# Kernel tuning notes

Measured on AMD Instinct MI355X. Metric: run time of the kernel, lower is better.

## Reference

```python
import jax, jax.numpy as jnp
import numpy as np

EPS = 1e-5
NEIGHBOR_K = 3
NEG_SLOPE = 0.2

def _conv(x, w):
    # x: [N,C,H,W], w: [O,I,3,3], stride 1, SAME padding
    return jax.lax.conv_general_dilated(
        x, w, window_strides=(1, 1), padding='SAME',
        dimension_numbers=('NCHW', 'OIHW', 'NCHW'))

def _bn(x, gamma, beta):
    # BatchNorm2d in training mode: batch statistics over (N,H,W), biased var
    m = x.mean(axis=(0, 2, 3), keepdims=True)
    v = x.var(axis=(0, 2, 3), keepdims=True)
    xn = (x - m) * jax.lax.rsqrt(v + EPS)
    return xn * gamma.reshape(1, -1, 1, 1) + beta.reshape(1, -1, 1, 1)

def _lrelu(x):
    return jnp.where(x >= 0, x, NEG_SLOPE * x)

def _maxpool2(x):
    return jax.lax.reduce_window(x, -jnp.inf, jax.lax.max,
                                 (1, 1, 2, 2), (1, 1, 2, 2), 'VALID')

def _features(x, w1, g1, b1, w2, g2, b2, w3, g3, b3, w4, g4, b4):
    x = _maxpool2(_lrelu(_bn(_conv(x, w1), g1, b1)))
    x = _maxpool2(_lrelu(_bn(_conv(x, w2), g2, b2)))
    x = _lrelu(_bn(_conv(x, w3), g3, b3))
    x = _lrelu(_bn(_conv(x, w4), g4, b4))
    return x  # [N, 64, 21, 21]

def setup_inputs() -> dict:
    key = jax.random.key(0)
    ks = jax.random.split(key, 8)
    inp = {
        'input1': jax.random.normal(ks[0], (32, 3, 84, 84), jnp.float32),
        'input2': jax.random.normal(ks[1], (5, 5, 3, 84, 84), jnp.float32),
        'w1': jax.random.normal(ks[2], (64, 3, 3, 3), jnp.float32) * 0.1,
        'g1': jax.random.uniform(ks[3], (64,), jnp.float32, 0.5, 1.5),
        'b1': jnp.zeros((64,), jnp.float32),
        'w2': jax.random.normal(ks[4], (64, 64, 3, 3), jnp.float32) * 0.1,
        'g2': jax.random.uniform(ks[5], (64,), jnp.float32, 0.5, 1.5),
        'b2': jnp.zeros((64,), jnp.float32),
        'w3': jax.random.normal(ks[6], (64, 64, 3, 3), jnp.float32) * 0.1,
        'g3': jax.random.uniform(ks[7], (64,), jnp.float32, 0.5, 1.5),
        'b3': jnp.zeros((64,), jnp.float32),
        'w4': jax.random.normal(jax.random.fold_in(key, 100), (64, 64, 3, 3), jnp.float32) * 0.1,
        'g4': jax.random.uniform(jax.random.fold_in(key, 101), (64,), jnp.float32, 0.5, 1.5),
        'b4': jnp.zeros((64,), jnp.float32),
    }
    return inp

def reference(input1, input2, w1, g1, b1, w2, g2, b2, w3, g3, b3, w4, g4, b4):
    params = (w1, g1, b1, w2, g2, b2, w3, g3, b3, w4, g4, b4)
    # Query features: [B, C, h, w]
    q = _features(input1, *params)
    B, C, h, w = q.shape
    hw = h * w
    Q = q.reshape(B, C, hw).transpose(0, 2, 1)            # [B, hw, C]
    qn = jnp.linalg.norm(Q, axis=2, keepdims=True)        # [B, hw, 1]
    # Support features, BN stats per class-batch (matches per-class forward)
    s = jax.vmap(lambda x: _features(x, *params))(input2) # [nc, shot, C, h, w]
    nc, shot = s.shape[0], s.shape[1]
    S = s.transpose(0, 2, 1, 3, 4).reshape(nc, C, shot * hw)  # [nc, C, M]
    sn = jnp.linalg.norm(S, axis=1, keepdims=True)            # [nc, 1, M]
    # Cosine similarities: [B, nc, hw, M]
    sims = jnp.einsum('bqc,ncm->bnqm', Q, S)
    sims = sims / (qn[:, None, :, :] * sn[None, :, :, :])
    topv = jax.lax.top_k(sims, NEIGHBOR_K)[0]              # [B, nc, hw, k]
    return topv.sum(axis=(2, 3))                           # [B, nc]
```

## Files before the change

kernel.cpp:

```cpp
#include <hip/hip_runtime.h>
#include <hip/hip_bf16.h>
#include <stdint.h>

#define NQ 32
#define NCLS 5
#define SHOT 5
#define NIMG 57
#define P1 7056
#define P2 1764
#define P3 441
#define PX 3528
#define MM (SHOT*P3)
#define EPSB 1e-5f
#define SLOPE 0.2f
#define NEGINF -3.4e38f
#define NREP 32
#define MSPAN 576
#define MRNG 4
#define SLS 88

typedef __attribute__((ext_vector_type(8))) short short8;
typedef __attribute__((ext_vector_type(4))) float f32x4;

__device__ __forceinline__ unsigned short bf16bits(float v)
{
    __hip_bfloat16 h = __float2bfloat16(v);
    return *reinterpret_cast<unsigned short*>(&h);
}
__device__ __forceinline__ float bits2f(unsigned short u)
{
    unsigned int x = ((unsigned int)u) << 16;
    return *reinterpret_cast<float*>(&x);
}

__global__ void pack_all_k(const float* __restrict__ w1, const float* __restrict__ w2,
                           const float* __restrict__ w3, const float* __restrict__ w4,
                           unsigned short* __restrict__ wpk1, unsigned short* __restrict__ wpk2,
                           unsigned short* __restrict__ wpk3, unsigned short* __restrict__ wpk4,
                           float* __restrict__ sums)
{
    int i = blockIdx.x * 256 + threadIdx.x;
    if (i < 4 * 6 * 64 * 2 * NREP) sums[i] = 0.f;
    if (i < 3 * 36864) {
        int set = i / 36864, ii = i - set * 36864;
        const float* w = (set == 0) ? w2 : (set == 1) ? w3 : w4;
        unsigned short* wpk = (set == 0) ? wpk2 : (set == 1) ? wpk3 : wpk4;
        int j = ii & 7, lane = (ii >> 3) & 63, chunk = ii >> 9;
        int nt = chunk & 3, half = (chunk >> 2) & 1, t = chunk >> 3;
        int co = nt * 16 + (lane & 15);
        int ci = half * 32 + (lane >> 4) * 8 + j;
        wpk[ii] = bf16bits(w[co * 576 + ci * 9 + t]);
    } else {
        int ii = i - 3 * 36864;
        if (ii >= 4096) return;
        int j = ii & 7, lane = (ii >> 3) & 63, c8 = ii >> 9;
        int nt = c8 & 3, f = c8 >> 2;
        int co = nt * 16 + (lane & 15), q = lane >> 4;
        int k = q * 8 + j;
        float val = 0.f;
        if (f == 0) {
            int t = k >> 2, ci = k & 3;
            if (ci < 3) val = w1[co * 27 + ci * 9 + t];
        } else if (k < 4) {
            int ci = k & 3;
            if (ci < 3) val = w1[co * 27 + ci * 9 + 8];
        }
        wpk1[ii] = bf16bits(val);
    }
}

__global__ __launch_bounds__(256) void conv1m_k(const float* __restrict__ in1,
                                                const float* __restrict__ in2,
                                                const unsigned short* __restrict__ wpk1,
                                                __hip_bfloat16* __restrict__ xpool,
                                                float* __restrict__ sums)
{
    constexpr int S = 84, P = P1, MBLK = 256, NB = 28, SPAN = MBLK + 2 * S + 2;
    __shared__ __align__(16) unsigned short ls4[SPAN * 4];
    __shared__ float qs[4][64], qs2[4][64];
    int img = blockIdx.x / NB;
    int p0 = (blockIdx.x % NB) * MBLK;
    int tid = threadIdx.x, lane = tid & 63, wv = tid >> 6;
    int col = lane & 15, quad = lane >> 4;
    const float* in = (img < NQ) ? in1 + (size_t)img * 3 * P1
                                 : in2 + (size_t)(img - NQ) * 3 * P1;
    for (int u = tid; u < SPAN; u += 256) {
        int p = p0 - S - 1 + u;
        union { unsigned short us[4]; uint2 u2; } o;
        o.u2 = (uint2){0u, 0u};
        if (p >= 0 && p < P) {
            o.us[0] = bf16bits(in[p]);
            o.us[1] = bf16bits(in[P1 + p]);
            o.us[2] = bf16bits(in[2 * P1 + p]);
        }
        *(uint2*)(ls4 + u * 4) = o.u2;
    }
    const short8* wb = (const short8*)wpk1;
    short8 b0[4], b1[4];
    #pragma unroll
    for (int nt = 0; nt < 4; ++nt) {
        b0[nt] = wb[(size_t)(nt * 64 + lane)];
        b1[nt] = wb[(size_t)((4 + nt) * 64 + lane)];
    }
    int t0 = 2 * quad, t1 = t0 + 1;
    int d0 = (t0 / 3 - 1) * S + (t0 % 3 - 1);
    int d1 = (t1 / 3 - 1) * S + (t1 % 3 - 1);
    const int d8 = S + 1;
    int tx0 = t0 % 3, tx1 = t1 % 3;
    __syncthreads();
    f32x4 acc[4][4];
    #pragma unroll
    for (int mt = 0; mt < 4; ++mt)
        #pragma unroll
        for (int nt = 0; nt < 4; ++nt) acc[mt][nt] = (f32x4){0.f, 0.f, 0.f, 0.f};
    #pragma unroll
    for (int mt = 0; mt < 4; ++mt) {
        int pl = wv * 64 + mt * 16 + col;
        int xm = (p0 + pl) % S;
        int base = pl + S + 1;
        uint2 h0 = *(const uint2*)(ls4 + (base + d0) * 4);
        uint2 h1 = *(const uint2*)(ls4 + (base + d1) * 4);
        uint2 h8 = *(const uint2*)(ls4 + (base + d8) * 4);
        bool ok0 = (tx0 == 0) ? (xm >= 1) : ((tx0 == 2) ? (xm <= S - 2) : true);
        bool ok1 = (tx1 == 0) ? (xm >= 1) : ((tx1 == 2) ? (xm <= S - 2) : true);
        bool ok8 = (quad == 0) && (xm <= S - 2);
        if (!ok0) h0 = (uint2){0u, 0u};
        if (!ok1) h1 = (uint2){0u, 0u};
        if (!ok8) h8 = (uint2){0u, 0u};
        union { uint4 u; short8 s; } ca, cb;
        ca.u = (uint4){h0.x, h0.y, h1.x, h1.y};
        cb.u = (uint4){h8.x, h8.y, 0u, 0u};
        #pragma unroll
        for (int nt = 0; nt < 4; ++nt) {
            acc[mt][nt] = __builtin_amdgcn_mfma_f32_16x16x32_bf16(ca.s, b0[nt], acc[mt][nt], 0, 0, 0);
            acc[mt][nt] = __builtin_amdgcn_mfma_f32_16x16x32_bf16(cb.s, b1[nt], acc[mt][nt], 0, 0, 0);
        }
    }
    float s[4] = {0.f, 0.f, 0.f, 0.f}, s2[4] = {0.f, 0.f, 0.f, 0.f};
    __hip_bfloat16* ob = xpool + (size_t)img * PX * 64;
    #pragma unroll
    for (int mt = 0; mt < 4; ++mt) {
        int tb = p0 + wv * 64 + mt * 16 + quad * 4;
        #pragma unroll
        for (int reg = 0; reg < 4; ++reg) {
            int pr = tb + reg;
            if (pr < P) {
                #pragma unroll
                for (int nt = 0; nt < 4; ++nt) {
                    float v = acc[mt][nt][reg];
                    s[nt] += v;
                    s2[nt] = fmaf(v, v, s2[nt]);
                }
            }
        }
        #pragma unroll
        for (int pr2 = 0; pr2 < 2; ++pr2) {
            int m0 = tb + pr2 * 2;
            if (m0 < P) {
                #pragma unroll
                for (int nt = 0; nt < 4; ++nt) {
                    float v = fmaxf(acc[mt][nt][pr2 * 2], acc[mt][nt][pr2 * 2 + 1]);
                    ob[(size_t)(m0 >> 1) * 64 + nt * 16 + col] = __float2bfloat16(v);
                }
            }
        }
    }
    #pragma unroll
    for (int d = 16; d < 64; d <<= 1)
        #pragma unroll
        for (int nt = 0; nt < 4; ++nt) {
            s[nt] += __shfl_xor(s[nt], d, 64);
            s2[nt] += __shfl_xor(s2[nt], d, 64);
        }
    if (quad == 0) {
        #pragma unroll
        for (int nt = 0; nt < 4; ++nt) {
            qs[wv][nt * 16 + col] = s[nt];
            qs2[wv][nt * 16 + col] = s2[nt];
        }
    }
    __syncthreads();
    if (wv == 0) {
        int g = (img < NQ) ? 0 : 1 + (img - NQ) / SHOT;
        int rep = blockIdx.x & (NREP - 1);
        float ts = qs[0][lane] + qs[1][lane] + qs[2][lane] + qs[3][lane];
        float ts2 = qs2[0][lane] + qs2[1][lane] + qs2[2][lane] + qs2[3][lane];
        float* base = sums + ((size_t)(g * 64 + lane) * 2) * NREP + rep;
        atomicAdd(base, ts);
        atomicAdd(base + NREP, ts2);
    }
}

template <int S, int MBLK, int MODE, bool POOLX>
__global__ __launch_bounds__(256) void conv64m_k(const unsigned short* __restrict__ inv,
                                                 const unsigned short* __restrict__ wpk,
                                                 __hip_bfloat16* __restrict__ out,
                                                 float* __restrict__ sums,
                                                 const float* __restrict__ msin)
{
    constexpr int P = S * S;
    constexpr int MT = MBLK / 64;
    constexpr int NB = (P + MBLK - 1) / MBLK;
    constexpr int SPAN = MBLK + 2 * S + 2;
    __shared__ __align__(16) unsigned short ls[SPAN * 72];
    __shared__ float qs[4][64], qs2[4][64];
    int img = blockIdx.x / NB;
    int p0 = (blockIdx.x % NB) * MBLK;
    int tid = threadIdx.x;
    int lane = tid & 63, wv = tid >> 6;
    int col = lane & 15, quad = lane >> 4;
    int g = (img < NQ) ? 0 : 1 + (img - NQ) / SHOT;
    if constexpr (MODE == 0) {
        const unsigned short* ib = inv + (size_t)img * P * 64;
        for (int u = tid; u < SPAN * 8; u += 256) {
            int pix = u >> 3, part = u & 7;
            int p = p0 - S - 1 + pix;
            short8 v = {0, 0, 0, 0, 0, 0, 0, 0};
            if (p >= 0 && p < P) v = *(const short8*)(ib + (size_t)p * 64 + part * 8);
            *(short8*)(ls + pix * 72 + part * 8) = v;
        }
    } else {
        int part = tid & 7;
        float ba[8], bb[8];
        #pragma unroll
        for (int j = 0; j < 8; ++j) {
            float2 ab = ((const float2*)msin)[g * 64 + part * 8 + j];
            ba[j] = ab.x;
            bb[j] = ab.y;
        }
        if constexpr (MODE == 1) {
            const unsigned short* ib = inv + (size_t)img * P * 64;
            for (int u = tid; u < SPAN * 8; u += 256) {
                int pix = u >> 3;
                int p = p0 - S - 1 + pix;
                union { unsigned short us[8]; short8 s8; } o;
                #pragma unroll
                for (int j = 0; j < 8; ++j) o.us[j] = 0;
                if (p >= 0 && p < P) {
                    union { short8 s8; unsigned short us[8]; } x;
                    x.s8 = *(const short8*)(ib + (size_t)p * 64 + part * 8);
                    #pragma unroll
                    for (int j = 0; j < 8; ++j) {
                        float v = fmaf(bits2f(x.us[j]), ba[j], bb[j]);
                        v = fmaxf(v, SLOPE * v);
                        o.us[j] = bf16bits(v);
                    }
                }
                *(short8*)(ls + pix * 72 + part * 8) = o.s8;
            }
        } else {
            const unsigned short* ib2 = inv + (size_t)img * (2 * (size_t)P) * 64;
            for (int u = tid; u < SPAN * 8; u += 256) {
                int pix = u >> 3;
                int p = p0 - S - 1 + pix;
                union { unsigned short us[8]; short8 s8; } o;
                #pragma unroll
                for (int j = 0; j < 8; ++j) o.us[j] = 0;
                if (p >= 0 && p < P) {
                    int y = p / S, x = p - y * S;
                    const unsigned short* src = ib2 + ((size_t)(2 * y) * S + x) * 64 + part * 8;
                    union { short8 s8; unsigned short us[8]; } x0, x1;
                    x0.s8 = *(const short8*)src;
                    x1.s8 = *(const short8*)(src + (size_t)S * 64);
                    #pragma unroll
                    for (int j = 0; j < 8; ++j) {
                        float v = fmaxf(bits2f(x0.us[j]), bits2f(x1.us[j]));
                        v = fmaf(v, ba[j], bb[j]);
                        v = fmaxf(v, SLOPE * v);
                        o.us[j] = bf16bits(v);
                    }
                }
                *(short8*)(ls + pix * 72 + part * 8) = o.s8;
            }
        }
    }
    __syncthreads();
    f32x4 acc[MT][4];
    #pragma unroll
    for (int mt = 0; mt < MT; ++mt)
        #pragma unroll
        for (int nt = 0; nt < 4; ++nt) acc[mt][nt] = (f32x4){0.f, 0.f, 0.f, 0.f};
    bool mok0[MT], mok2[MT];
    #pragma unroll
    for (int mt = 0; mt < MT; ++mt) {
        int xm = (p0 + wv * (MT * 16) + mt * 16 + col) % S;
        mok0[mt] = xm >= 1;
        mok2[mt] = xm <= S - 2;
    }
    const short8* wb = (const short8*)wpk;
    #pragma unroll
    for (int ky = 0; ky < 3; ++ky) {
        #pragma unroll
        for (int kx = 0; kx < 3; ++kx) {
            int t = ky * 3 + kx;
            int d = (ky - 1) * S + (kx - 1);
            #pragma unroll
            for (int half = 0; half < 2; ++half) {
                short8 b[4];
                #pragma unroll
                for (int nt = 0; nt < 4; ++nt)
                    b[nt] = wb[((t * 2 + half) * 4 + nt) * 64 + lane];
                #pragma unroll
                for (int mt = 0; mt < MT; ++mt) {
                    int idx = wv * (MT * 16) + mt * 16 + col + S + 1 + d;
                    short8 a = *(const short8*)(ls + idx * 72 + half * 32 + quad * 8);
                    bool ok = (kx == 0) ? mok0[mt] : (kx == 2) ? mok2[mt] : true;
                    if (!ok) a = (short8){0, 0, 0, 0, 0, 0, 0, 0};
                    #pragma unroll
                    for (int nt = 0; nt < 4; ++nt)
                        acc[mt][nt] = __builtin_amdgcn_mfma_f32_16x16x32_bf16(a, b[nt], acc[mt][nt], 0, 0, 0);
                }
            }
        }
    }
    float s[4] = {0.f, 0.f, 0.f, 0.f}, s2[4] = {0.f, 0.f, 0.f, 0.f};
    __hip_bfloat16* ob = out + (size_t)img * (POOLX ? P / 2 : P) * 64;
    #pragma unroll
    for (int mt = 0; mt < MT; ++mt) {
        int tb = p0 + wv * (MT * 16) + mt * 16 + quad * 4;
        #pragma unroll
        for (int reg = 0; reg < 4; ++reg) {
            int pr = tb + reg;
            if (pr < P) {
                #pragma unroll
                for (int nt = 0; nt < 4; ++nt) {
                    float v = acc[mt][nt][reg];
                    s[nt] += v;
                    s2[nt] = fmaf(v, v, s2[nt]);
                }
            }
        }
        if constexpr (POOLX) {
            #pragma unroll
            for (int pr2 = 0; pr2 < 2; ++pr2) {
                int m0 = tb + pr2 * 2;
                if (m0 < P) {
                    #pragma unroll
                    for (int nt = 0; nt < 4; ++nt) {
                        float v = fmaxf(acc[mt][nt][pr2 * 2], acc[mt][nt][pr2 * 2 + 1]);
                        ob[(size_t)(m0 >> 1) * 64 + nt * 16 + col] = __float2bfloat16(v);
                    }
                }
            }
        } else {
            #pragma unroll
            for (int reg = 0; reg < 4; ++reg) {
                int pr = tb + reg;
                if (pr < P) {
                    #pragma unroll
                    for (int nt = 0; nt < 4; ++nt)
                        ob[(size_t)pr * 64 + nt * 16 + col] = __float2bfloat16(acc[mt][nt][reg]);
                }
            }
        }
    }
    #pragma unroll
    for (int d = 16; d < 64; d <<= 1)
        #pragma unroll
        for (int nt = 0; nt < 4; ++nt) {
            s[nt] += __shfl_xor(s[nt], d, 64);
            s2[nt] += __shfl_xor(s2[nt], d, 64);
        }
    if (quad == 0) {
        #pragma unroll
        for (int nt = 0; nt < 4; ++nt) {
            qs[wv][nt * 16 + col] = s[nt];
            qs2[wv][nt * 16 + col] = s2[nt];
        }
    }
    __syncthreads();
    if (wv == 0) {
        int rep = blockIdx.x & (NREP - 1);
        float ts = qs[0][lane] + qs[1][lane] + qs[2][lane] + qs[3][lane];
        float ts2 = qs2[0][lane] + qs2[1][lane] + qs2[2][lane] + qs2[3][lane];
        float* base = sums + ((size_t)(g * 64 + lane) * 2) * NREP + rep;
        atomicAdd(base, ts);
        atomicAdd(base + NREP, ts2);
    }
}

__global__ void finalize_k(const float* __restrict__ sums, float* __restrict__ ms,
                           const float* __restrict__ gamma, const float* __restrict__ beta, int P)
{
    int i = blockIdx.x * blockDim.x + threadIdx.x;
    if (i >= 6 * 64) return;
    int g = i >> 6, c = i & 63;
    const float* ps = sums + (size_t)i * 2 * NREP;
    float s = 0.f, s2 = 0.f;
    #pragma unroll
    for (int r = 0; r < NREP; ++r) { s += ps[r]; s2 += ps[NREP + r]; }
    float cnt = (float)((g == 0 ? NQ : SHOT) * P);
    float mean = s / cnt;
    float var = s2 / cnt - mean * mean;
    float a = rsqrtf(var + EPSB) * gamma[c];
    ms[i * 2] = a;
    ms[i * 2 + 1] = fmaf(-mean, a, beta[c]);
}

__global__ __launch_bounds__(256) void bnnorm_k(const unsigned short* __restrict__ x,
                                                const float* __restrict__ ms,
                                                __hip_bfloat16* __restrict__ out)
{
    int lane = threadIdx.x & 63, wvr = threadIdx.x >> 6;
    int pix = blockIdx.x * 4 + wvr;
    if (pix >= NIMG * P3) return;
    int img = pix / P3;
    int g = (img < NQ) ? 0 : 1 + (img - NQ) / SHOT;
    float v = fmaf(bits2f(x[(size_t)pix * 64 + lane]), ms[(g * 64 + lane) * 2], ms[(g * 64 + lane) * 2 + 1]);
    v = v >= 0.f ? v : SLOPE * v;
    float ss = v * v;
    #pragma unroll
    for (int d = 32; d > 0; d >>= 1) ss += __shfl_xor(ss, d, 64);
    out[(size_t)pix * 64 + lane] = __float2bfloat16(v * rsqrtf(ss));
}

__device__ __forceinline__ void ins3(float v, float& t0, float& t1, float& t2)
{
    float n1 = __builtin_amdgcn_fmed3f(v, t0, t1);
    float n2 = __builtin_amdgcn_fmed3f(v, t1, t2);
    t0 = fmaxf(t0, v);
    t1 = n1;
    t2 = n2;
}

__global__ __launch_bounds__(256, 6) void sim_part_k(const __hip_bfloat16* __restrict__ fhat,
                                                     float* __restrict__ part)
{
    __shared__ __align__(16) unsigned short sl[64 * SLS];
    int t = blockIdx.x;
    int mr = t & 3;
    int qb = (t >> 2) % 7;
    int n = (t / 28) % NCLS;
    int bq = t / (28 * NCLS);
    int tid = threadIdx.x, lane = tid & 63, wv = tid >> 6;
    int col = lane & 15, quad = lane >> 4;
    int q = qb * 64 + wv * 16 + col;
    int qc = q < P3 ? q : P3 - 1;
    const unsigned short* qp = (const unsigned short*)fhat + ((size_t)bq * P3 + qc) * 64;
    short8 a0 = *(const short8*)(qp + quad * 8);
    short8 a1 = *(const short8*)(qp + 32 + quad * 8);
    const unsigned short* sp = (const unsigned short*)fhat + (size_t)(NQ + n * SHOT) * P3 * 64;
    int m_lo = mr * MSPAN;
    int m_cnt = MM - m_lo; if (m_cnt > MSPAN) m_cnt = MSPAN;
    int nch = (m_cnt + 63) >> 6;
    float t0[4], t1[4], t2[4];
    #pragma unroll
    for (int r = 0; r < 4; ++r) { t0[r] = NEGINF; t1[r] = NEGINF; t2[r] = NEGINF; }
    int srow = tid >> 3, scc = (tid & 7) * 8;
    for (int c = 0; c < nch; ++c) {
        int m0 = m_lo + c * 64;
        __syncthreads();
        #pragma unroll
        for (int pass = 0; pass < 2; ++pass) {
            int row = srow + pass * 32;
            int m = m0 + row;
            short8 vv = {0, 0, 0, 0, 0, 0, 0, 0};
            if (m < MM) vv = *(const short8*)(sp + (size_t)m * 64 + scc);
            *(short8*)(sl + row * SLS + scc) = vv;
        }
        __syncthreads();
        const unsigned short* sr = sl + col * SLS + quad * 8;
        #pragma unroll
        for (int mt = 0; mt < 4; ++mt) {
            if (m0 + mt * 16 < MM) {
                short8 b0 = *(const short8*)(sr);
                short8 b1 = *(const short8*)(sr + 32);
                f32x4 acc = {0.f, 0.f, 0.f, 0.f};
                acc = __builtin_amdgcn_mfma_f32_16x16x32_bf16(a0, b0, acc, 0, 0, 0);
                acc = __builtin_amdgcn_mfma_f32_16x16x32_bf16(a1, b1, acc, 0, 0, 0);
                #pragma unroll
                for (int r = 0; r < 4; ++r) ins3(acc[r], t0[r], t1[r], t2[r]);
            }
            sr += 16 * SLS;
        }
    }
    #pragma unroll
    for (int d = 1; d < 16; d <<= 1)
        #pragma unroll
        for (int r = 0; r < 4; ++r) {
            float u0 = __shfl_xor(t0[r], d, 64);
            float u1 = __shfl_xor(t1[r], d, 64);
            float u2 = __shfl_xor(t2[r], d, 64);
            ins3(u0, t0[r], t1[r], t2[r]);
            ins3(u1, t0[r], t1[r], t2[r]);
            ins3(u2, t0[r], t1[r], t2[r]);
        }
    if (col == 0) {
        #pragma unroll
        for (int r = 0; r < 4; ++r) {
            int ql = wv * 16 + quad * 4 + r;
            float* pp = part + ((((size_t)(bq * NCLS + n) * 7 + qb) * 4 + mr) * 64 + ql) * 3;
            pp[0] = t0[r];
            pp[1] = t1[r];
            pp[2] = t2[r];
        }
    }
}

__global__ __launch_bounds__(256) void sim_merge_k(const float* __restrict__ part,
                                                   float* __restrict__ out)
{
    __shared__ float red[4];
    int b = blockIdx.x;
    int tid = threadIdx.x, lane = tid & 63, wv = tid >> 6;
    float s = 0.f;
    for (int q = tid; q < P3; q += 256) {
        int qb = q >> 6, ql = q & 63;
        const float* pp = part + (((size_t)b * 7 + qb) * 4 * 64 + ql) * 3;
        float v0 = pp[0], v1 = pp[1], v2 = pp[2];
        #pragma unroll
        for (int mr = 1; mr < 4; ++mr) {
            const float* pm = pp + (size_t)mr * 192;
            ins3(pm[0], v0, v1, v2);
            ins3(pm[1], v0, v1, v2);
            ins3(pm[2], v0, v1, v2);
        }
        s += v0 + v1 + v2;
    }
    #pragma unroll
    for (int d = 32; d > 0; d >>= 1) s += __shfl_xor(s, d, 64);
    if (lane == 0) red[wv] = s;
    __syncthreads();
    if (tid == 0) out[b] = red[0] + red[1] + red[2] + red[3];
}

extern "C" void kernel_launch(void* const* d_in, const int* in_sizes, int n_in,
                              void* d_out, int out_size, void* d_ws, size_t ws_size,
                              hipStream_t stream)
{
    const float* input1 = (const float*)d_in[0];
    const float* input2 = (const float*)d_in[1];
    const float* w1 = (const float*)d_in[2];
    const float* g1 = (const float*)d_in[3];
    const float* b1 = (const float*)d_in[4];
    const float* w2 = (const float*)d_in[5];
    const float* g2 = (const float*)d_in[6];
    const float* b2 = (const float*)d_in[7];
    const float* w3 = (const float*)d_in[8];
    const float* g3 = (const float*)d_in[9];
    const float* b3 = (const float*)d_in[10];
    const float* w4 = (const float*)d_in[11];
    const float* g4 = (const float*)d_in[12];
    const float* b4 = (const float*)d_in[13];
    float* out = (float*)d_out;

    char* w8 = (char*)d_ws;
    const size_t oB = 51480576;
    const size_t oT = oB + 12870144;
    const size_t STG = 6 * 64 * 2 * NREP * sizeof(float);
    __hip_bfloat16* xpool1 = (__hip_bfloat16*)(w8 + 0);
    __hip_bfloat16* conv3raw = (__hip_bfloat16*)(w8 + 0);
    __hip_bfloat16* conv4raw = (__hip_bfloat16*)(w8 + 9652608);
    __hip_bfloat16* fhat = (__hip_bfloat16*)(w8 + 16087680);
    __hip_bfloat16* xpool2 = (__hip_bfloat16*)(w8 + oB);
    float* sums = (float*)(w8 + oT);
    float* ms = (float*)(w8 + oT + 4 * STG);
    unsigned short* wpk2 = (unsigned short*)(w8 + oT + 4 * STG + 12288);
    unsigned short* wpk3 = (unsigned short*)(w8 + oT + 4 * STG + 12288 + 73728);
    unsigned short* wpk4 = (unsigned short*)(w8 + oT + 4 * STG + 12288 + 147456);
    unsigned short* wpk1 = (unsigned short*)(w8 + oT + 4 * STG + 12288 + 221184);
    const size_t oP = oT + 4 * STG + 12288 + 221184 + 8192;
    float* part = (float*)(w8 + oP);
    if (ws_size < oP + (size_t)NQ * NCLS * 7 * MRNG * 64 * 3 * sizeof(float)) return;
    float* sums1 = sums;
    float* sums2 = sums + 6 * 64 * 2 * NREP;
    float* sums3 = sums2 + 6 * 64 * 2 * NREP;
    float* sums4 = sums3 + 6 * 64 * 2 * NREP;

    pack_all_k<<<448, 256, 0, stream>>>(w1, w2, w3, w4, wpk1, wpk2, wpk3, wpk4, sums);

    conv1m_k<<<NIMG * 28, 256, 0, stream>>>(input1, input2, wpk1, xpool1, sums1);
    finalize_k<<<2, 256, 0, stream>>>(sums1, ms + 0, g1, b1, P1);
    conv64m_k<42, 256, 2, true><<<NIMG * 7, 256, 0, stream>>>(
        (const unsigned short*)xpool1, wpk2, xpool2, sums2, ms + 0);
    finalize_k<<<2, 256, 0, stream>>>(sums2, ms + 768, g2, b2, P2);
    conv64m_k<21, 128, 2, false><<<NIMG * 4, 256, 0, stream>>>(
        (const unsigned short*)xpool2, wpk3, conv3raw, sums3, ms + 768);
    finalize_k<<<2, 256, 0, stream>>>(sums3, ms + 1536, g3, b3, P3);
    conv64m_k<21, 128, 1, false><<<NIMG * 4, 256, 0, stream>>>(
        (const unsigned short*)conv3raw, wpk4, conv4raw, sums4, ms + 1536);
    finalize_k<<<2, 256, 0, stream>>>(sums4, ms + 2304, g4, b4, P3);
    bnnorm_k<<<6285, 256, 0, stream>>>((const unsigned short*)conv4raw, ms + 2304, fhat);
    sim_part_k<<<NQ * NCLS * 7 * MRNG, 256, 0, stream>>>(fhat, part);
    sim_merge_k<<<NQ * NCLS, 256, 0, stream>>>(part, out);
}
```

Measured before the change: 222.0 us.

## Widen similarity query tile to 128 rows, prefetch support chunks, swizzle top-k merge

The similarity kernel now gives each wave two 16-row query groups (128 queries per block instead of 64). Each support tile loaded into LDS therefore feeds twice as many MFMAs, and there are fewer blocks (4 query blocks instead of 7). Support rows for the next chunk are prefetched into registers while the current chunk is computed, and the LDS row stride shrinks to 72. The cross-lane top-3 merge switches from shfl_xor to ds_swizzle, and ins3 drops two temporaries. Register pressure rises (launch bound goes from 6 to 5 waves), and the last query block pads 128 rows for only 441 queries.

Result: no change. 224.2 us (+1.0%).

```diff
diff --git a/kernel.cpp b/kernel.cpp
--- a/kernel.cpp
+++ b/kernel.cpp
@@ -17,7 +17,9 @@
 #define NREP 32
 #define MSPAN 576
 #define MRNG 4
-#define SLS 88
+#define QBLK 128
+#define NQB 4
+#define SLS 72
 
 typedef __attribute__((ext_vector_type(8))) short short8;
 typedef __attribute__((ext_vector_type(4))) float f32x4;
@@ -416,84 +418,109 @@
 
 __device__ __forceinline__ void ins3(float v, float& t0, float& t1, float& t2)
 {
-    float n1 = __builtin_amdgcn_fmed3f(v, t0, t1);
-    float n2 = __builtin_amdgcn_fmed3f(v, t1, t2);
+    t2 = __builtin_amdgcn_fmed3f(v, t1, t2);
+    t1 = __builtin_amdgcn_fmed3f(v, t0, t1);
     t0 = fmaxf(t0, v);
-    t1 = n1;
-    t2 = n2;
-}
-
-__global__ __launch_bounds__(256, 6) void sim_part_k(const __hip_bfloat16* __restrict__ fhat,
+}
+
+template <int PAT>
+__device__ __forceinline__ void swzmerge(float& t0, float& t1, float& t2)
+{
+    float u0 = __int_as_float(__builtin_amdgcn_ds_swizzle(__float_as_int(t0), PAT));
+    float u1 = __int_as_float(__builtin_amdgcn_ds_swizzle(__float_as_int(t1), PAT));
+    float u2 = __int_as_float(__builtin_amdgcn_ds_swizzle(__float_as_int(t2), PAT));
+    ins3(u0, t0, t1, t2);
+    ins3(u1, t0, t1, t2);
+    ins3(u2, t0, t1, t2);
+}
+
+__global__ __launch_bounds__(256, 5) void sim_part_k(const __hip_bfloat16* __restrict__ fhat,
                                                      float* __restrict__ part)
 {
     __shared__ __align__(16) unsigned short sl[64 * SLS];
     int t = blockIdx.x;
     int mr = t & 3;
-    int qb = (t >> 2) % 7;
-    int n = (t / 28) % NCLS;
-    int bq = t / (28 * NCLS);
+    int qb = (t >> 2) & 3;
+    int n = (t >> 4) % NCLS;
+    int bq = t / (16 * NCLS);
     int tid = threadIdx.x, lane = tid & 63, wv = tid >> 6;
     int col = lane & 15, quad = lane >> 4;
-    int q = qb * 64 + wv * 16 + col;
-    int qc = q < P3 ? q : P3 - 1;
-    const unsigned short* qp = (const unsigned short*)fhat + ((size_t)bq * P3 + qc) * 64;
-    short8 a0 = *(const short8*)(qp + quad * 8);
-    short8 a1 = *(const short8*)(qp + 32 + quad * 8);
+    short8 a0[2], a1[2];
+    #pragma unroll
+    for (int g = 0; g < 2; ++g) {
+        int q = qb * QBLK + wv * 32 + g * 16 + col;
+        int qc = q < P3 ? q : P3 - 1;
+        const unsigned short* qp = (const unsigned short*)fhat + ((size_t)bq * P3 + qc) * 64;
+        a0[g] = *(const short8*)(qp + quad * 8);
+        a1[g] = *(const short8*)(qp + 32 + quad * 8);
+    }
     const unsigned short* sp = (const unsigned short*)fhat + (size_t)(NQ + n * SHOT) * P3 * 64;
     int m_lo = mr * MSPAN;
     int m_cnt = MM - m_lo; if (m_cnt > MSPAN) m_cnt = MSPAN;
     int nch = (m_cnt + 63) >> 6;
-    float t0[4], t1[4], t2[4];
-    #pragma unroll
-    for (int r = 0; r < 4; ++r) { t0[r] = NEGINF; t1[r] = NEGINF; t2[r] = NEGINF; }
+    float t0[2][4], t1[2][4], t2[2][4];
+    #pragma unroll
+    for (int g = 0; g < 2; ++g)
+        #pragma unroll
+        for (int r = 0; r < 4; ++r) { t0[g][r] = NEGINF; t1[g][r] = NEGINF; t2[g][r] = NEGINF; }
     int srow = tid >> 3, scc = (tid & 7) * 8;
+    const unsigned short* gp = sp + (size_t)(m_lo + srow) * 64 + scc;
+    unsigned short* ld0 = sl + srow * SLS + scc;
+    const unsigned short* sr = sl + col * SLS + quad * 8;
+    int mcur = m_lo + srow;
+    const short8 z8 = {0, 0, 0, 0, 0, 0, 0, 0};
+    short8 v0 = z8, v1 = z8;
+    if (mcur < MM) v0 = *(const short8*)gp;
+    if (mcur + 32 < MM) v1 = *(const short8*)(gp + 32 * 64);
     for (int c = 0; c < nch; ++c) {
+        __syncthreads();
+        *(short8*)ld0 = v0;
+        *(short8*)(ld0 + 32 * SLS) = v1;
+        __syncthreads();
+        if (c + 1 < nch) {
+            gp += 64 * 64;
+            mcur += 64;
+            v0 = z8; v1 = z8;
+            if (mcur < MM) v0 = *(const short8*)gp;
+            if (mcur + 32 < MM) v1 = *(const short8*)(gp + 32 * 64);
+        }
         int m0 = m_lo + c * 64;
-        __syncthreads();
-        #pragma unroll
-        for (int pass = 0; pass < 2; ++pass) {
-            int row = srow + pass * 32;
-            int m = m0 + row;
-            short8 vv = {0, 0, 0, 0, 0, 0, 0, 0};
-            if (m < MM) vv = *(const short8*)(sp + (size_t)m * 64 + scc);
-            *(short8*)(sl + row * SLS + scc) = vv;
-        }
-        __syncthreads();
-        const unsigned short* sr = sl + col * SLS + quad * 8;
         #pragma unroll
         for (int mt = 0; mt < 4; ++mt) {
             if (m0 + mt * 16 < MM) {
-                short8 b0 = *(const short8*)(sr);
-                short8 b1 = *(const short8*)(sr + 32);
-                f32x4 acc = {0.f, 0.f, 0.f, 0.f};
-                acc = __builtin_amdgcn_mfma_f32_16x16x32_bf16(a0, b0, acc, 0, 0, 0);
-                acc = __builtin_amdgcn_mfma_f32_16x16x32_bf16(a1, b1, acc, 0, 0, 0);
-                #pragma unroll
-                for (int r = 0; r < 4; ++r) ins3(acc[r], t0[r], t1[r], t2[r]);
-            }
-            sr += 16 * SLS;
-        }
-    }
-    #pragma unroll
-    for (int d = 1; d < 16; d <<= 1)
+                short8 b0 = *(const short8*)(sr + mt * (16 * SLS));
+                short8 b1 = *(const short8*)(sr + mt * (16 * SLS) + 32);
+                #pragma unroll
+                for (int g = 0; g < 2; ++g) {
+                    f32x4 acc = {0.f, 0.f, 0.f, 0.f};
+                    acc = __builtin_amdgcn_mfma_f32_16x16x32_bf16(a0[g], b0, acc, 0, 0, 0);
+                    acc = __builtin_amdgcn_mfma_f32_16x16x32_bf16(a1[g], b1, acc, 0, 0, 0);
+                    #pragma unroll
+                    for (int r = 0; r < 4; ++r) ins3(acc[r], t0[g][r], t1[g][r], t2[g][r]);
+                }
+            }
+        }
+    }
+    #pragma unroll
+    for (int g = 0; g < 2; ++g)
         #pragma unroll
         for (int r = 0; r < 4; ++r) {
-            float u0 = __shfl_xor(t0[r], d, 64);
-            float u1 = __shfl_xor(t1[r], d, 64);
-            float u2 = __shfl_xor(t2[r], d, 64);
-            ins3(u0, t0[r], t1[r], t2[r]);
-            ins3(u1, t0[r], t1[r], t2[r]);
-            ins3(u2, t0[r], t1[r], t2[r]);
+            swzmerge<0x041F>(t0[g][r], t1[g][r], t2[g][r]);
+            swzmerge<0x081F>(t0[g][r], t1[g][r], t2[g][r]);
+            swzmerge<0x101F>(t0[g][r], t1[g][r], t2[g][r]);
+            swzmerge<0x201F>(t0[g][r], t1[g][r], t2[g][r]);
         }
     if (col == 0) {
         #pragma unroll
-        for (int r = 0; r < 4; ++r) {
-            int ql = wv * 16 + quad * 4 + r;
-            float* pp = part + ((((size_t)(bq * NCLS + n) * 7 + qb) * 4 + mr) * 64 + ql) * 3;
-            pp[0] = t0[r];
-            pp[1] = t1[r];
-            pp[2] = t2[r];
-        }
+        for (int g = 0; g < 2; ++g)
+            #pragma unroll
+            for (int r = 0; r < 4; ++r) {
+                int ql = wv * 32 + g * 16 + quad * 4 + r;
+                float* pp = part + ((((size_t)(bq * NCLS + n) * NQB + qb) * MRNG + mr) * QBLK + ql) * 3;
+                pp[0] = t0[g][r];
+                pp[1] = t1[g][r];
+                pp[2] = t2[g][r];
+            }
     }
 }
 
@@ -505,12 +532,12 @@
     int tid = threadIdx.x, lane = tid & 63, wv = tid >> 6;
     float s = 0.f;
     for (int q = tid; q < P3; q += 256) {
-        int qb = q >> 6, ql = q & 63;
-        const float* pp = part + (((size_t)b * 7 + qb) * 4 * 64 + ql) * 3;
+        int qb = q >> 7, ql = q & 127;
+        const float* pp = part + (((size_t)b * NQB + qb) * MRNG * QBLK + ql) * 3;
         float v0 = pp[0], v1 = pp[1], v2 = pp[2];
         #pragma unroll
         for (int mr = 1; mr < 4; ++mr) {
-            const float* pm = pp + (size_t)mr * 192;
+            const float* pm = pp + (size_t)mr * (QBLK * 3);
             ins3(pm[0], v0, v1, v2);
             ins3(pm[1], v0, v1, v2);
             ins3(pm[2], v0, v1, v2);
@@ -561,7 +588,7 @@
     unsigned short* wpk1 = (unsigned short*)(w8 + oT + 4 * STG + 12288 + 221184);
     const size_t oP = oT + 4 * STG + 12288 + 221184 + 8192;
     float* part = (float*)(w8 + oP);
-    if (ws_size < oP + (size_t)NQ * NCLS * 7 * MRNG * 64 * 3 * sizeof(float)) return;
+    if (ws_size < oP + (size_t)NQ * NCLS * NQB * MRNG * QBLK * 3 * sizeof(float)) return;
     float* sums1 = sums;
     float* sums2 = sums + 6 * 64 * 2 * NREP;
     float* sums3 = sums2 + 6 * 64 * 2 * NREP;
@@ -581,6 +608,6 @@
         (const unsigned short*)conv3raw, wpk4, conv4raw, sums4, ms + 1536);
     finalize_k<<<2, 256, 0, stream>>>(sums4, ms + 2304, g4, b4, P3);
     bnnorm_k<<<6285, 256, 0, stream>>>((const unsigned short*)conv4raw, ms + 2304, fhat);
-    sim_part_k<<<NQ * NCLS * 7 * MRNG, 256, 0, stream>>>(fhat, part);
+    sim_part_k<<<NQ * NCLS * NQB * MRNG, 256, 0, stream>>>(fhat, part);
     sim_merge_k<<<NQ * NCLS, 256, 0, stream>>>(part, out);
 }
```
